# Optimization experiments

Hardware: AMD Instinct MI355X
Metric: run time of the kernel (lower is better)

Reference implementation:

```python
import jax, jax.numpy as jnp
import numpy as np

N_NODES = 100000
N_EDGES = 3200000


def _norm_weights(edge_index, n):
    # Append self loops (GCNConv gcn_norm adds them back after the module's A - I)
    loops = jnp.arange(n, dtype=edge_index.dtype)
    row = jnp.concatenate([edge_index[0], loops])
    col = jnp.concatenate([edge_index[1], loops])
    ones = jnp.ones(row.shape[0], dtype=jnp.float32)
    deg = jax.ops.segment_sum(ones, row, num_segments=n)
    dinv = jnp.where(deg > 0, jax.lax.rsqrt(deg), 0.0)
    w = dinv[row] * dinv[col]  # symmetric normalization D^-1/2 (A+I) D^-1/2
    return row, col, w


def _spmm(row, col, w, h, n):
    # out[i] = sum_{(i,j) in E} w_ij * h[j]
    return jax.ops.segment_sum(w[:, None] * h[col], row, num_segments=n)


def setup_inputs() -> dict:
    key = jax.random.key(0)
    ks = jax.random.split(key, 4)
    x = jax.random.normal(ks[0], (N_NODES, 512), dtype=jnp.float32)
    W1 = jax.random.normal(ks[1], (512, 16), dtype=jnp.float32) * (1.0 / np.sqrt(512))
    b1 = jnp.zeros((16,), dtype=jnp.float32)
    W2 = jax.random.normal(ks[2], (16, 40), dtype=jnp.float32) * (1.0 / np.sqrt(16))
    b2 = jnp.zeros((40,), dtype=jnp.float32)
    edge_index = jax.random.randint(ks[3], (2, N_EDGES), 0, N_NODES, dtype=jnp.int64)
    return {"x": x, "W1": W1, "b1": b1, "W2": W2, "b2": b2, "edge_index": edge_index}


def reference(x, W1, b1, W2, b2, edge_index):
    n = x.shape[0]
    row, col, w = _norm_weights(edge_index, n)
    # GCNConv layer 1: A_norm @ (x W1) + b1, then relu (dropout is identity in eval)
    h = _spmm(row, col, w, x @ W1, n) + b1
    h = jax.nn.relu(h)
    # GCNConv layer 2 (same adjacency: adj2 is a clone of adj1)
    out = _spmm(row, col, w, h @ W2, n) + b2
    return jax.nn.log_softmax(out, axis=1)
```

## Files before the change

kernel.cpp:

```cpp
#include <hip/hip_runtime.h>
#include <hip/hip_fp16.h>
#include <math.h>

#define F0 512
#define F1 16
#define F2 40
#define CB_SHIFT 8
#define CB_ROWS 256
#define NCB_MAX 512
#define CAPCB 9216
#define EPB 8192
#define COL_BITS 17
#define CMASK ((1 << COL_BITS) - 1)
#define CNT_STRIDE 16

__global__ void k_zero(int* p, int m) {
    int i = blockIdx.x * blockDim.x + threadIdx.x;
    if (i < m) p[i] = 0;
}

__global__ __launch_bounds__(512) void k_fill(const int* __restrict__ row,
                                              const int* __restrict__ col, int E,
                                              int* cnt, int* __restrict__ ebuf,
                                              int NCB) {
    __shared__ int hcnt[NCB_MAX];
    __shared__ int lexcl[NCB_MAX];
    __shared__ int hbase[NCB_MAX];
    __shared__ int part[NCB_MAX];
    __shared__ int sorted[EPB];
    int t = threadIdx.x;
    int e0 = blockIdx.x * EPB;
    int nloc = min(EPB, E - e0);
    if (t < NCB_MAX) hcnt[t] = 0;
    __syncthreads();

    int rr[16], cc[16];
#pragma unroll
    for (int k = 0; k < 4; k++) {
        int base = t * 4 + k * 2048;
        if (base + 3 < nloc) {
            int4 r4 = *(const int4*)(row + e0 + base);
            int4 c4 = *(const int4*)(col + e0 + base);
            rr[k * 4 + 0] = r4.x; rr[k * 4 + 1] = r4.y;
            rr[k * 4 + 2] = r4.z; rr[k * 4 + 3] = r4.w;
            cc[k * 4 + 0] = c4.x; cc[k * 4 + 1] = c4.y;
            cc[k * 4 + 2] = c4.z; cc[k * 4 + 3] = c4.w;
        } else {
#pragma unroll
            for (int q = 0; q < 4; q++) {
                int e = base + q;
                rr[k * 4 + q] = (e < nloc) ? row[e0 + e] : -1;
                cc[k * 4 + q] = (e < nloc) ? col[e0 + e] : 0;
            }
        }
    }
#pragma unroll
    for (int q = 0; q < 16; q++)
        if (rr[q] >= 0) atomicAdd(&hcnt[rr[q] >> CB_SHIFT], 1);
    __syncthreads();
    int myv = hcnt[t];
    part[t] = myv;
    __syncthreads();
    for (int off = 1; off < NCB_MAX; off <<= 1) {
        int a = (t >= off) ? part[t - off] : 0;
        __syncthreads();
        part[t] += a;
        __syncthreads();
    }
    lexcl[t] = part[t] - myv;
    hbase[t] = (myv > 0) ? atomicAdd(&cnt[t * CNT_STRIDE], myv) : 0;
    hcnt[t] = 0;
    __syncthreads();
#pragma unroll
    for (int q = 0; q < 16; q++) {
        int r = rr[q];
        if (r >= 0) {
            int cb = r >> CB_SHIFT;
            int p = lexcl[cb] + atomicAdd(&hcnt[cb], 1);
            sorted[p] = ((r & (CB_ROWS - 1)) << COL_BITS) | cc[q];
        }
    }
    __syncthreads();
    int wv = t >> 6, lane = t & 63;
    for (int cb = wv; cb < NCB; cb += 8) {
        int c = hcnt[cb];
        int ls = lexcl[cb];
        int* dst = ebuf + (size_t)cb * CAPCB + hbase[cb];
        for (int j = lane; j < c; j += 64) dst[j] = sorted[ls + j];
    }
}

__global__ __launch_bounds__(512) void k_scan2(const int* __restrict__ cnt, int NCB,
                                               int* __restrict__ sbbase) {
    __shared__ int part[NCB_MAX];
    int t = threadIdx.x;
    int v = (t < NCB) ? cnt[t * CNT_STRIDE] : 0;
    part[t] = v;
    __syncthreads();
    for (int off = 1; off < NCB_MAX; off <<= 1) {
        int a = (t >= off) ? part[t - off] : 0;
        __syncthreads();
        part[t] += a;
        __syncthreads();
    }
    if (t < NCB) sbbase[t] = part[t] - v;
}

__global__ __launch_bounds__(256) void k_sort(const int* __restrict__ cnt,
                                              const int* __restrict__ sbbase,
                                              const int* __restrict__ ebuf, int n,
                                              int* __restrict__ colsort,
                                              int* __restrict__ deg,
                                              int* __restrict__ rs,
                                              float* __restrict__ dinv) {
    __shared__ int rcnt[CB_ROWS];
    __shared__ int rexcl[CB_ROWS];
    __shared__ int sorted[CAPCB];
    int cb = blockIdx.x;
    int t = threadIdx.x;
    int c = cnt[cb * CNT_STRIDE];
    const int* seg = ebuf + (size_t)cb * CAPCB;
    rcnt[t] = 0;
    __syncthreads();
    for (int base = t * 4; base < c; base += 1024) {
        if (base + 3 < c) {
            int4 v = *(const int4*)(seg + base);
            atomicAdd(&rcnt[v.x >> COL_BITS], 1);
            atomicAdd(&rcnt[v.y >> COL_BITS], 1);
            atomicAdd(&rcnt[v.z >> COL_BITS], 1);
            atomicAdd(&rcnt[v.w >> COL_BITS], 1);
        } else {
            for (int k = base; k < c; k++) atomicAdd(&rcnt[seg[k] >> COL_BITS], 1);
        }
    }
    __syncthreads();
    int myc = rcnt[t];
    rexcl[t] = myc;
    __syncthreads();
    for (int off = 1; off < CB_ROWS; off <<= 1) {
        int a = (t >= off) ? rexcl[t - off] : 0;
        __syncthreads();
        rexcl[t] += a;
        __syncthreads();
    }
    int excl = rexcl[t] - myc;
    int gbase = sbbase[cb];
    int i = (cb << CB_SHIFT) + t;
    if (i < n) {
        deg[i] = myc;
        rs[i] = gbase + excl;
        dinv[i] = rsqrtf((float)(myc + 1));
    }
    rcnt[t] = excl;
    __syncthreads();
    for (int base = t * 4; base < c; base += 1024) {
        if (base + 3 < c) {
            int4 v = *(const int4*)(seg + base);
            int p0 = atomicAdd(&rcnt[v.x >> COL_BITS], 1); sorted[p0] = v.x & CMASK;
            int p1 = atomicAdd(&rcnt[v.y >> COL_BITS], 1); sorted[p1] = v.y & CMASK;
            int p2 = atomicAdd(&rcnt[v.z >> COL_BITS], 1); sorted[p2] = v.z & CMASK;
            int p3 = atomicAdd(&rcnt[v.w >> COL_BITS], 1); sorted[p3] = v.w & CMASK;
        } else {
            for (int k = base; k < c; k++) {
                int v = seg[k];
                int p = atomicAdd(&rcnt[v >> COL_BITS], 1);
                sorted[p] = v & CMASK;
            }
        }
    }
    __syncthreads();
    for (int j = t; j < c; j += 256) colsort[gbase + j] = sorted[j];
}

__global__ __launch_bounds__(256, 2) void k_gemm1(const float* __restrict__ x,
                                                  const float* __restrict__ W1,
                                                  const float* __restrict__ dinv,
                                                  __half* __restrict__ hp, int n,
                                                  int total_waves) {
    int lane = threadIdx.x & 63;
    int wid = blockIdx.x * (blockDim.x >> 6) + (threadIdx.x >> 6);

    float w[8][16];
#pragma unroll
    for (int h = 0; h < 2; h++) {
#pragma unroll
        for (int r = 0; r < 4; r++) {
            int k = h * 256 + 4 * lane + r;
            const float4* p = (const float4*)(W1 + k * 16);
            float4 a = p[0], b = p[1], c = p[2], d = p[3];
            float* wr = w[h * 4 + r];
            wr[0] = a.x; wr[1] = a.y; wr[2] = a.z; wr[3] = a.w;
            wr[4] = b.x; wr[5] = b.y; wr[6] = b.z; wr[7] = b.w;
            wr[8] = c.x; wr[9] = c.y; wr[10] = c.z; wr[11] = c.w;
            wr[12] = d.x; wr[13] = d.y; wr[14] = d.z; wr[15] = d.w;
        }
    }

    for (int i0 = wid * 4; i0 < n; i0 += total_waves * 4) {
        float4 xq[8];
        if (i0 + 3 < n) {
            const float4* xp = (const float4*)(x + (size_t)i0 * F0);
#pragma unroll
            for (int q = 0; q < 8; q++) xq[q] = xp[q * 64 + lane];
        } else {
#pragma unroll
            for (int q = 0; q < 8; q++) {
                int r = q >> 1;
                if (i0 + r < n) {
                    const float4* xp = (const float4*)(x + (size_t)(i0 + r) * F0);
                    xq[q] = xp[(q & 1) * 64 + lane];
                } else {
                    xq[q] = make_float4(0.f, 0.f, 0.f, 0.f);
                }
            }
        }
        bool b0 = (lane & 1) != 0;
        bool b1 = (lane & 2) != 0;
        bool b2 = (lane & 4) != 0;
        bool b3 = (lane & 8) != 0;
#pragma unroll
        for (int r = 0; r < 4; r++) {
            float4 xa = xq[2 * r], xb = xq[2 * r + 1];
            float v16[16];
#pragma unroll
            for (int j = 0; j < 16; j++) {
                v16[j] = xa.x * w[0][j] + xa.y * w[1][j] + xa.z * w[2][j] + xa.w * w[3][j]
                       + xb.x * w[4][j] + xb.y * w[5][j] + xb.z * w[6][j] + xb.w * w[7][j];
            }
            float v8[8];
#pragma unroll
            for (int t2 = 0; t2 < 8; t2++) {
                float a = v16[2 * t2], b = v16[2 * t2 + 1];
                float keep = b0 ? b : a;
                float send = b0 ? a : b;
                v8[t2] = keep + __shfl_xor(send, 1);
            }
            float v4[4];
#pragma unroll
            for (int t2 = 0; t2 < 4; t2++) {
                float a = v8[2 * t2], b = v8[2 * t2 + 1];
                float keep = b1 ? b : a;
                float send = b1 ? a : b;
                v4[t2] = keep + __shfl_xor(send, 2);
            }
            float v2[2];
#pragma unroll
            for (int t2 = 0; t2 < 2; t2++) {
                float a = v4[2 * t2], b = v4[2 * t2 + 1];
                float keep = b2 ? b : a;
                float send = b2 ? a : b;
                v2[t2] = keep + __shfl_xor(send, 4);
            }
            float keep = b3 ? v2[1] : v2[0];
            float send = b3 ? v2[0] : v2[1];
            float v1 = keep + __shfl_xor(send, 8);
            v1 += __shfl_xor(v1, 16);
            v1 += __shfl_xor(v1, 32);
            int i = i0 + r;
            if (lane < 16 && i < n)
                hp[(size_t)i * F1 + lane] = __float2half_rn(dinv[i] * v1);
        }
    }
}

__global__ __launch_bounds__(256) void k_spmm1(const __half* __restrict__ hp,
                                               const int* __restrict__ rs,
                                               const int* __restrict__ deg,
                                               const int* __restrict__ colsort,
                                               const float* __restrict__ dinv,
                                               const float* __restrict__ b1,
                                               __half* __restrict__ s2, int n) {
    int t = threadIdx.x;
    int jq = t & 3;
    int i = blockIdx.x * 64 + (t >> 2);
    if (i >= n) return;
    int s = rs[i], c = deg[i];
    const int* cs = colsort + s;

    float4 acc;
    {
        float2 r = *(const float2*)(hp + (size_t)i * F1 + 4 * jq);
        __half2 h01 = *(__half2*)&r.x;
        __half2 h23 = *(__half2*)&r.y;
        float2 f01 = __half22float2(h01), f23 = __half22float2(h23);
        acc = make_float4(f01.x, f01.y, f23.x, f23.y);
    }
    int e = 0;
    for (; e + 7 < c; e += 8) {
        int cc[8];
#pragma unroll
        for (int q = 0; q < 8; q++) cc[q] = cs[e + q];
        float2 rr[8];
#pragma unroll
        for (int q = 0; q < 8; q++)
            rr[q] = *(const float2*)(hp + (size_t)cc[q] * F1 + 4 * jq);
#pragma unroll
        for (int q = 0; q < 8; q++) {
            __half2 h01 = *(__half2*)&rr[q].x;
            __half2 h23 = *(__half2*)&rr[q].y;
            float2 f01 = __half22float2(h01), f23 = __half22float2(h23);
            acc.x += f01.x; acc.y += f01.y; acc.z += f23.x; acc.w += f23.y;
        }
    }
    for (; e < c; e++) {
        float2 r = *(const float2*)(hp + (size_t)cs[e] * F1 + 4 * jq);
        __half2 h01 = *(__half2*)&r.x;
        __half2 h23 = *(__half2*)&r.y;
        float2 f01 = __half22float2(h01), f23 = __half22float2(h23);
        acc.x += f01.x; acc.y += f01.y; acc.z += f23.x; acc.w += f23.y;
    }
    float di = dinv[i];
    float4 bb = *(const float4*)(b1 + 4 * jq);
    float h0 = fmaxf(di * acc.x + bb.x, 0.f);
    float h1 = fmaxf(di * acc.y + bb.y, 0.f);
    float h2 = fmaxf(di * acc.z + bb.z, 0.f);
    float h3 = fmaxf(di * acc.w + bb.w, 0.f);
    float2 ov;
    *(__half2*)&ov.x = __floats2half2_rn(di * h0, di * h1);
    *(__half2*)&ov.y = __floats2half2_rn(di * h2, di * h3);
    *(float2*)(s2 + (size_t)i * F1 + 4 * jq) = ov;
}

__global__ __launch_bounds__(256) void k_spmm2(const __half* __restrict__ s2,
                                               const int* __restrict__ rs,
                                               const int* __restrict__ deg,
                                               const int* __restrict__ colsort,
                                               const float* __restrict__ dinv,
                                               const float* __restrict__ W2,
                                               const float* __restrict__ b2,
                                               float* __restrict__ out, int n) {
    __shared__ float sW2[F1 * F2];
    int t = threadIdx.x;
    for (int idx = t; idx < F1 * F2; idx += 256) sW2[idx] = W2[idx];
    __syncthreads();

    int jh = t & 7;
    int i = blockIdx.x * 32 + (t >> 3);
    if (i >= n) return;
    int s = rs[i], c = deg[i];
    const int* cs = colsort + s;
    float2 acc = __half22float2(*(const __half2*)(s2 + (size_t)i * F1 + 2 * jh));
    int e = 0;
    for (; e + 7 < c; e += 8) {
        int cc[8];
#pragma unroll
        for (int q = 0; q < 8; q++) cc[q] = cs[e + q];
        __half2 hh[8];
#pragma unroll
        for (int q = 0; q < 8; q++)
            hh[q] = *(const __half2*)(s2 + (size_t)cc[q] * F1 + 2 * jh);
#pragma unroll
        for (int q = 0; q < 8; q++) {
            float2 f = __half22float2(hh[q]);
            acc.x += f.x; acc.y += f.y;
        }
    }
    for (; e < c; e++) {
        float2 f = __half22float2(*(const __half2*)(s2 + (size_t)cs[e] * F1 + 2 * jh));
        acc.x += f.x; acc.y += f.y;
    }
    float di = dinv[i];
    float zx0 = di * acc.x, zy0 = di * acc.y;

    float o[5] = {0.f, 0.f, 0.f, 0.f, 0.f};
#pragma unroll
    for (int sl = 0; sl < 8; sl++) {
        float zx = __shfl(zx0, sl, 8);
        float zy = __shfl(zy0, sl, 8);
#pragma unroll
        for (int q = 0; q < 5; q++) {
            int k = jh + 8 * q;
            o[q] += zx * sW2[(2 * sl) * F2 + k] + zy * sW2[(2 * sl + 1) * F2 + k];
        }
    }
    float v[5];
    float m = -INFINITY;
#pragma unroll
    for (int q = 0; q < 5; q++) {
        v[q] = o[q] + b2[jh + 8 * q];
        m = fmaxf(m, v[q]);
    }
#pragma unroll
    for (int off = 1; off < 8; off <<= 1) m = fmaxf(m, __shfl_xor(m, off, 8));
    float ssum = 0.f;
#pragma unroll
    for (int q = 0; q < 5; q++) ssum += __expf(v[q] - m);
#pragma unroll
    for (int off = 1; off < 8; off <<= 1) ssum += __shfl_xor(ssum, off, 8);
    float lse = m + __logf(ssum);
    float* orow = out + (size_t)i * F2;
#pragma unroll
    for (int q = 0; q < 5; q++) orow[jh + 8 * q] = v[q] - lse;
}

extern "C" void kernel_launch(void* const* d_in, const int* in_sizes, int n_in,
                              void* d_out, int out_size, void* d_ws, size_t ws_size,
                              hipStream_t stream) {
    const float* x  = (const float*)d_in[0];
    const float* W1 = (const float*)d_in[1];
    const float* b1 = (const float*)d_in[2];
    const float* W2 = (const float*)d_in[3];
    const float* b2 = (const float*)d_in[4];
    const int*   ei = (const int*)d_in[5];

    int n = in_sizes[0] / F0;
    int E = in_sizes[5] / 2;
    const int* row = ei;
    const int* col = ei + E;
    int NCB = (n + CB_ROWS - 1) >> CB_SHIFT;

    int* deg     = (int*)d_ws;
    int* rs      = deg + n;
    float* dinv  = (float*)(rs + n);
    int* cnt     = (int*)(dinv + n);
    int* sbbase  = cnt + NCB_MAX * CNT_STRIDE;
    int* colsort = sbbase + NCB_MAX;
    int* ebuf    = colsort + E;
    __half* hp   = (__half*)ebuf;
    __half* s2   = hp + (size_t)n * F1;

    int nchunks = (E + EPB - 1) / EPB;
    k_zero<<<(NCB * CNT_STRIDE + 255) / 256, 256, 0, stream>>>(cnt, NCB * CNT_STRIDE);
    k_fill<<<nchunks, 512, 0, stream>>>(row, col, E, cnt, ebuf, NCB);
    k_scan2<<<1, NCB_MAX, 0, stream>>>(cnt, NCB, sbbase);
    k_sort<<<NCB, 256, 0, stream>>>(cnt, sbbase, ebuf, n, colsort, deg, rs, dinv);

    int g1_blocks = 2048;
    k_gemm1<<<g1_blocks, 256, 0, stream>>>(x, W1, dinv, hp, n, g1_blocks * 4);
    k_spmm1<<<(n + 63) / 64, 256, 0, stream>>>(hp, rs, deg, colsort, dinv, b1, s2, n);
    k_spmm2<<<(n + 31) / 32, 256, 0, stream>>>(s2, rs, deg, colsort, dinv, W2, b2,
                                               (float*)d_out, n);
}
```

Baseline: 424.0 us.

## Bucket nodes by degree so SpMM waves process similar-degree rows

Adds three small kernels that histogram node degrees, scan the histogram, and build a permutation that groups nodes by degree. Both SpMM kernels then read rows through this permutation, so threads in a wave hold similar edge counts and suffer less load imbalance and divergence. The cost is three extra launches, an extra indirection per row, and scattered output writes that lose row locality.

```diff
diff --git a/kernel.cpp b/kernel.cpp
--- a/kernel.cpp
+++ b/kernel.cpp
@@ -13,6 +13,7 @@
 #define COL_BITS 17
 #define CMASK ((1 << COL_BITS) - 1)
 #define CNT_STRIDE 16
+#define DBINS 128
 
 __global__ void k_zero(int* p, int m) {
     int i = blockIdx.x * blockDim.x + threadIdx.x;
@@ -172,6 +173,68 @@
     for (int j = t; j < c; j += 256) colsort[gbase + j] = sorted[j];
 }
 
+__global__ __launch_bounds__(256) void k_dhist(const int* __restrict__ deg, int n,
+                                               int* __restrict__ dcnt) {
+    __shared__ int h[DBINS];
+    int t = threadIdx.x;
+    if (t < DBINS) h[t] = 0;
+    __syncthreads();
+    int base = blockIdx.x * 1024 + t * 4;
+#pragma unroll
+    for (int q = 0; q < 4; q++) {
+        int i = base + q;
+        if (i < n) atomicAdd(&h[min(deg[i], DBINS - 1)], 1);
+    }
+    __syncthreads();
+    if (t < DBINS && h[t] > 0) atomicAdd(&dcnt[t], h[t]);
+}
+
+__global__ __launch_bounds__(DBINS) void k_dscan(const int* __restrict__ dcnt,
+                                                 int* __restrict__ dcur) {
+    __shared__ int part[DBINS];
+    int t = threadIdx.x;
+    int v = dcnt[t];
+    part[t] = v;
+    __syncthreads();
+    for (int off = 1; off < DBINS; off <<= 1) {
+        int a = (t >= off) ? part[t - off] : 0;
+        __syncthreads();
+        part[t] += a;
+        __syncthreads();
+    }
+    dcur[t] = part[t] - v;
+}
+
+__global__ __launch_bounds__(256) void k_dperm(const int* __restrict__ deg, int n,
+                                               int* dcur, int* __restrict__ perm) {
+    __shared__ int lcnt[DBINS];
+    __shared__ int lbase[DBINS];
+    int t = threadIdx.x;
+    if (t < DBINS) lcnt[t] = 0;
+    __syncthreads();
+    int base = blockIdx.x * 1024 + t * 4;
+    int b[4];
+#pragma unroll
+    for (int q = 0; q < 4; q++) {
+        int i = base + q;
+        b[q] = (i < n) ? min(deg[i], DBINS - 1) : -1;
+        if (b[q] >= 0) atomicAdd(&lcnt[b[q]], 1);
+    }
+    __syncthreads();
+    if (t < DBINS) {
+        lbase[t] = (lcnt[t] > 0) ? atomicAdd(&dcur[t], lcnt[t]) : 0;
+        lcnt[t] = 0;
+    }
+    __syncthreads();
+#pragma unroll
+    for (int q = 0; q < 4; q++) {
+        if (b[q] >= 0) {
+            int p = lbase[b[q]] + atomicAdd(&lcnt[b[q]], 1);
+            perm[p] = base + q;
+        }
+    }
+}
+
 __global__ __launch_bounds__(256, 2) void k_gemm1(const float* __restrict__ x,
                                                   const float* __restrict__ W1,
                                                   const float* __restrict__ dinv,
@@ -269,11 +332,13 @@
                                                const int* __restrict__ colsort,
                                                const float* __restrict__ dinv,
                                                const float* __restrict__ b1,
+                                               const int* __restrict__ perm,
                                                __half* __restrict__ s2, int n) {
     int t = threadIdx.x;
     int jq = t & 3;
-    int i = blockIdx.x * 64 + (t >> 2);
-    if (i >= n) return;
+    int ii = blockIdx.x * 64 + (t >> 2);
+    if (ii >= n) return;
+    int i = perm[ii];
     int s = rs[i], c = deg[i];
     const int* cs = colsort + s;
 
@@ -328,6 +393,7 @@
                                                const float* __restrict__ dinv,
                                                const float* __restrict__ W2,
                                                const float* __restrict__ b2,
+                                               const int* __restrict__ perm,
                                                float* __restrict__ out, int n) {
     __shared__ float sW2[F1 * F2];
     int t = threadIdx.x;
@@ -335,8 +401,9 @@
     __syncthreads();
 
     int jh = t & 7;
-    int i = blockIdx.x * 32 + (t >> 3);
-    if (i >= n) return;
+    int ii = blockIdx.x * 32 + (t >> 3);
+    if (ii >= n) return;
+    int i = perm[ii];
     int s = rs[i], c = deg[i];
     const int* cs = colsort + s;
     float2 acc = __half22float2(*(const __half2*)(s2 + (size_t)i * F1 + 2 * jh));
@@ -414,20 +481,30 @@
     float* dinv  = (float*)(rs + n);
     int* cnt     = (int*)(dinv + n);
     int* sbbase  = cnt + NCB_MAX * CNT_STRIDE;
-    int* colsort = sbbase + NCB_MAX;
+    int* dcnt    = sbbase + NCB_MAX;
+    int* dcur    = dcnt + DBINS;
+    int* perm    = dcur + DBINS;
+    int* colsort = perm + n;
     int* ebuf    = colsort + E;
     __half* hp   = (__half*)ebuf;
     __half* s2   = hp + (size_t)n * F1;
 
     int nchunks = (E + EPB - 1) / EPB;
+    int nrb = (n + 1023) / 1024;
     k_zero<<<(NCB * CNT_STRIDE + 255) / 256, 256, 0, stream>>>(cnt, NCB * CNT_STRIDE);
+    k_zero<<<1, 256, 0, stream>>>(dcnt, 2 * DBINS);
     k_fill<<<nchunks, 512, 0, stream>>>(row, col, E, cnt, ebuf, NCB);
     k_scan2<<<1, NCB_MAX, 0, stream>>>(cnt, NCB, sbbase);
     k_sort<<<NCB, 256, 0, stream>>>(cnt, sbbase, ebuf, n, colsort, deg, rs, dinv);
 
+    k_dhist<<<nrb, 256, 0, stream>>>(deg, n, dcnt);
+    k_dscan<<<1, DBINS, 0, stream>>>(dcnt, dcur);
+    k_dperm<<<nrb, 256, 0, stream>>>(deg, n, dcur, perm);
+
     int g1_blocks = 2048;
     k_gemm1<<<g1_blocks, 256, 0, stream>>>(x, W1, dinv, hp, n, g1_blocks * 4);
-    k_spmm1<<<(n + 63) / 64, 256, 0, stream>>>(hp, rs, deg, colsort, dinv, b1, s2, n);
+    k_spmm1<<<(n + 63) / 64, 256, 0, stream>>>(hp, rs, deg, colsort, dinv, b1, perm,
+                                               s2, n);
     k_spmm2<<<(n + 31) / 32, 256, 0, stream>>>(s2, rs, deg, colsort, dinv, W2, b2,
-                                               (float*)d_out, n);
-}
+                                               perm, (float*)d_out, n);
+}
```

Result: slower. 444.2 us (+4.8%).
